# Performance work log

Hardware: AMD Instinct MI355X
Metric: run time of the kernel (lower is better)

The kernel has to match this reference:

```python
import jax, jax.numpy as jnp
import numpy as np

N = 100000
IN_DIM = 256
HID = 128
E = 1600000


def _gcn_conv(x, W, b, src, dst, n_nodes):
    """PyG GCNConv: add self-loops, symmetric normalization, linear transform."""
    xw = x @ W  # [N, H]
    loop = jnp.arange(n_nodes, dtype=src.dtype)
    s = jnp.concatenate([src, loop])  # sources (j)
    d = jnp.concatenate([dst, loop])  # targets (i)
    ones = jnp.ones(s.shape[0], dtype=x.dtype)
    deg = jax.ops.segment_sum(ones, d, num_segments=n_nodes)  # in-degree incl. self-loop
    dinv = jnp.where(deg > 0, jax.lax.rsqrt(deg), 0.0)
    norm = dinv[s] * dinv[d]  # [E+N]
    msgs = xw[s] * norm[:, None]  # gather + scale
    out = jax.ops.segment_sum(msgs, d, num_segments=n_nodes)  # scatter-add at targets
    return out + b


def setup_inputs() -> dict:
    key = jax.random.key(0)
    ks = jax.random.split(key, 12)
    x = jax.random.normal(ks[0], (N, IN_DIM), dtype=jnp.float32)
    edge_index = jax.random.randint(ks[1], (2, E), 0, N, dtype=jnp.int64)
    h_node = jax.random.uniform(ks[2], (N,), dtype=jnp.float32)
    # learned params (glorot-ish scale)
    W1 = jax.random.normal(ks[3], (IN_DIM, HID), dtype=jnp.float32) / np.sqrt(IN_DIM)
    b1 = jnp.zeros((HID,), dtype=jnp.float32)
    W2 = jax.random.normal(ks[4], (HID, HID), dtype=jnp.float32) / np.sqrt(HID)
    b2 = jnp.zeros((HID,), dtype=jnp.float32)
    Wc = jax.random.normal(ks[5], (HID, 2), dtype=jnp.float32) / np.sqrt(HID)
    bc = jnp.zeros((2,), dtype=jnp.float32)
    Wf = jax.random.normal(ks[6], (HID, 2), dtype=jnp.float32) / np.sqrt(HID)
    bf = jnp.zeros((2,), dtype=jnp.float32)
    return {"x": x, "edge_index": edge_index, "h_node": h_node,
            "W1": W1, "b1": b1, "W2": W2, "b2": b2,
            "Wc": Wc, "bc": bc, "Wf": Wf, "bf": bf}


def reference(x, edge_index, h_node, W1, b1, W2, b2, Wc, bc, Wf, bf):
    src, dst = edge_index[0], edge_index[1]
    h1 = jax.nn.relu(_gcn_conv(x, W1, b1, src, dst, x.shape[0]))      # [N, HID]
    logits_coarse = h1 @ Wc + bc                                      # [N, 2]
    alpha = h_node[:, None]                                           # [N, 1]
    h2 = jax.nn.relu(_gcn_conv(h1, W2, b2, src, dst, x.shape[0]))     # [N, HID]
    h2_adaptive = alpha * h2 + (1.0 - alpha) * h1
    logits_fine = h2_adaptive @ Wf + bf                               # [N, 2]
    return 0.5 * logits_coarse + 0.5 * logits_fine
```

## Files before the change

### kernel.cpp

```cpp
#include <hip/hip_runtime.h>


#define HID 128
#define SHIFT 9
#define RANGE 512
#define MAXB 256
#define TILE 4096

typedef __bf16 bf16x8 __attribute__((ext_vector_type(8)));
typedef float  f32x4  __attribute__((ext_vector_type(4)));

__device__ __forceinline__ unsigned short f2bf(float x) {
    unsigned int b = __float_as_uint(x);
    b += 0x7fffu + ((b >> 16) & 1u);
    return (unsigned short)(b >> 16);
}
__device__ __forceinline__ float bflo(unsigned int u) { return __uint_as_float(u << 16); }
__device__ __forceinline__ float bfhi(unsigned int u) { return __uint_as_float(u & 0xffff0000u); }
__device__ __forceinline__ unsigned packbf(float a, float b) {
    return (unsigned)f2bf(a) | ((unsigned)f2bf(b) << 16);
}

__device__ __forceinline__ void gload_lds16(const void* g, void* l) {
    __builtin_amdgcn_global_load_lds(
        (const __attribute__((address_space(1))) void*)g,
        (__attribute__((address_space(3))) void*)l, 16, 0, 0);
}


__global__ __launch_bounds__(256)
void bincount_kernel(const int* __restrict__ dst, int* __restrict__ bin_counts,
                     int E, int NB) {
    __shared__ int h[MAXB];
    for (int i = threadIdx.x; i < NB; i += 256) h[i] = 0;
    __syncthreads();
    const int base = blockIdx.x * TILE;
#pragma unroll
    for (int j = 0; j < TILE; j += 256) {
        int e = base + j + threadIdx.x;
        if (e < E) atomicAdd(&h[((unsigned)dst[e]) >> SHIFT], 1);
    }
    __syncthreads();
    for (int i = threadIdx.x; i < NB; i += 256) {
        int v = h[i];
        if (v) atomicAdd(&bin_counts[i], v);
    }
}

__global__ void binscan_kernel(const int* __restrict__ bin_counts,
                               int* __restrict__ bin_off, int* __restrict__ bin_cur, int NB) {
    __shared__ int sh[MAXB];
    const int t = threadIdx.x;
    int v = (t < NB) ? bin_counts[t] : 0;
    sh[t] = v;
    __syncthreads();
    for (int s = 1; s < 256; s <<= 1) {
        int x = (t >= s) ? sh[t - s] : 0;
        __syncthreads();
        sh[t] += x;
        __syncthreads();
    }
    if (t < NB) {
        int ex = sh[t] - v;
        bin_off[t] = ex;
        bin_cur[t] = ex;
    }
}

__global__ __launch_bounds__(256)
void stage_kernel(const int* __restrict__ src, const int* __restrict__ dst,
                  int* __restrict__ bin_cur, unsigned* __restrict__ pairs, int E) {
    __shared__ int sh_hist[MAXB];
    __shared__ int sh_off[MAXB];
    __shared__ int sh_ex[MAXB];
    __shared__ int sh_gbase[MAXB];
    __shared__ uint2 stg[TILE];
    const int t = threadIdx.x;
    const int base = blockIdx.x * TILE;
    const int cnt = min(TILE, E - base);

    for (int i = t; i < MAXB; i += 256) sh_hist[i] = 0;
    __syncthreads();

    int s[16], d[16], r[16];
#pragma unroll
    for (int j = 0; j < 16; ++j) {
        const int k = j * 256 + t;
        if (k < cnt) {
            s[j] = src[base + k];
            d[j] = dst[base + k];
            r[j] = atomicAdd(&sh_hist[((unsigned)d[j]) >> SHIFT], 1);
        }
    }
    __syncthreads();

    const int hv = sh_hist[t];
    sh_off[t] = hv;
    __syncthreads();
    for (int st = 1; st < 256; st <<= 1) {
        int x = (t >= st) ? sh_off[t - st] : 0;
        __syncthreads();
        sh_off[t] += x;
        __syncthreads();
    }
    sh_ex[t] = sh_off[t] - hv;
    if (hv > 0) sh_gbase[t] = atomicAdd(&bin_cur[t], hv);
    __syncthreads();

#pragma unroll
    for (int j = 0; j < 16; ++j) {
        const int k = j * 256 + t;
        if (k < cnt) {
            int b = ((unsigned)d[j]) >> SHIFT;
            stg[sh_ex[b] + r[j]] = make_uint2((unsigned)s[j], (unsigned)d[j]);
        }
    }
    __syncthreads();

    for (int i = t; i < cnt; i += 256) {
        uint2 p = stg[i];
        int b = (int)(p.y >> SHIFT);
        unsigned w = ((p.y & (RANGE - 1)) << 23) | p.x;
        pairs[sh_gbase[b] + (i - sh_ex[b])] = w;
    }
}

__global__ __launch_bounds__(256)
void binrowp_kernel(const unsigned* __restrict__ pairs, const int* __restrict__ bin_off,
                    float* __restrict__ dinv, int* __restrict__ rowp,
                    int N, int NB, int E) {
    __shared__ int c[RANGE];
    __shared__ int sh[256];
    const int b = blockIdx.x;
    const int t = threadIdx.x;
    const int nb = b << SHIFT;
    const int nr = min(RANGE, N - nb);
    for (int i = t; i < RANGE; i += 256) c[i] = 0;
    __syncthreads();
    const int lo = bin_off[b];
    const int hi = (b + 1 < NB) ? bin_off[b + 1] : E;
    for (int i = lo + t; i < hi; i += 256)
        atomicAdd(&c[pairs[i] >> 23], 1);
    __syncthreads();
    const int v0 = c[2 * t], v1 = c[2 * t + 1];
    const int pr = v0 + v1;
    sh[t] = pr;
    __syncthreads();
    for (int s = 1; s < 256; s <<= 1) {
        int x = (t >= s) ? sh[t - s] : 0;
        __syncthreads();
        sh[t] += x;
        __syncthreads();
    }
    const int ex = sh[t] - pr + lo;
    if (2 * t < nr) {
        rowp[nb + 2 * t] = ex;
        dinv[nb + 2 * t] = rsqrtf((float)(v0 + 1));
    }
    if (2 * t + 1 < nr) {
        rowp[nb + 2 * t + 1] = ex + v0;
        dinv[nb + 2 * t + 1] = rsqrtf((float)(v1 + 1));
    }
    if (b == 0 && t == 0) rowp[N] = E;
}

__global__ __launch_bounds__(256)
void fine_kernel(const unsigned* __restrict__ pairs, const int* __restrict__ bin_off,
                 const int* __restrict__ rowp, const float* __restrict__ dinv,
                 uint2* __restrict__ colv2, int N, int NB, int E) {
    __shared__ int cur[RANGE];
    const int b = blockIdx.x;
    const int nb = b << SHIFT;
    const int nr = min(RANGE, N - nb);
    for (int i = threadIdx.x; i < nr; i += 256) cur[i] = rowp[nb + i];
    __syncthreads();
    const int lo = bin_off[b];
    const int hi = (b + 1 < NB) ? bin_off[b + 1] : E;
    for (int i = lo + threadIdx.x; i < hi; i += 256) {
        unsigned w = pairs[i];
        unsigned s = w & 0x7fffffu;
        int pos = atomicAdd(&cur[w >> 23], 1);
        colv2[pos] = make_uint2(s, __float_as_uint(dinv[s]));
    }
}

__global__ void wtprep_kernel(const float* __restrict__ W, unsigned short* __restrict__ Wt, int K) {
    int idx = blockIdx.x * 256 + threadIdx.x;
    if (idx < 128 * K) {
        int nn = idx / K, k = idx - nn * K;
        Wt[(size_t)nn * K + k] = f2bf(W[(size_t)k * 128 + nn]);
    }
}

template <bool A_BF16>
__global__ __launch_bounds__(256)
void gemm_kernel(const void* __restrict__ Aptr, const unsigned short* __restrict__ Wt,
                 unsigned short* __restrict__ Out, int nrows, int K) {
    __shared__ __align__(16) char tilebuf[16384];
    const int tid  = threadIdx.x;
    const int wave = tid >> 6;
    const int lane = tid & 63;
    const int q = lane >> 4;
    const int r = lane & 15;
    const int blkrow = blockIdx.x * 128;
    const int wrow = blkrow + wave * 32;

    f32x4 acc[2][8];
#pragma unroll
    for (int s = 0; s < 2; ++s)
#pragma unroll
        for (int c = 0; c < 8; ++c) acc[s][c] = (f32x4){0.f, 0.f, 0.f, 0.f};

    for (int k0 = 0; k0 < K; k0 += 32) {
        if (A_BF16) {
            const unsigned short* A = (const unsigned short*)Aptr;
#pragma unroll
            for (int c = 0; c < 2; ++c) {
                const int u = tid + c * 256;
                const int l = u & 63;
                const int g = u >> 6;
                int row = blkrow + (g >> 1) * 32 + (g & 1) * 16 + (l & 15);
                row = min(row, nrows - 1);
                const int k = k0 + (l >> 4) * 8;
                gload_lds16(A + (size_t)row * K + k,
                            tilebuf + c * 4096 + wave * 1024);
            }
        } else {
            const float* A = (const float*)Aptr;
#pragma unroll
            for (int c = 0; c < 4; ++c) {
                const int u = tid + c * 256;
                const int l = u & 63;
                const int g = u >> 6;
                const int half = g & 1;
                const int ws = g >> 1;
                int row = blkrow + (ws >> 1) * 32 + (ws & 1) * 16 + (l & 15);
                row = min(row, nrows - 1);
                const int k = k0 + (l >> 4) * 8 + half * 4;
                gload_lds16(A + (size_t)row * K + k,
                            tilebuf + c * 4096 + wave * 1024);
            }
        }
        __syncthreads();

        const int kk = k0 + q * 8;
        bf16x8 afrag[2];
#pragma unroll
        for (int s = 0; s < 2; ++s) {
            if (A_BF16) {
                afrag[s] = *reinterpret_cast<const bf16x8*>(
                    tilebuf + ((wave * 2 + s) * 64 + lane) * 16);
            } else {
                const float4 x0 = *reinterpret_cast<const float4*>(
                    tilebuf + (((wave * 2 + s) * 2 + 0) * 64 + lane) * 16);
                const float4 x1 = *reinterpret_cast<const float4*>(
                    tilebuf + (((wave * 2 + s) * 2 + 1) * 64 + lane) * 16);
                bf16x8 a;
                a[0] = (__bf16)x0.x; a[1] = (__bf16)x0.y; a[2] = (__bf16)x0.z; a[3] = (__bf16)x0.w;
                a[4] = (__bf16)x1.x; a[5] = (__bf16)x1.y; a[6] = (__bf16)x1.z; a[7] = (__bf16)x1.w;
                afrag[s] = a;
            }
        }
#pragma unroll
        for (int c = 0; c < 8; ++c) {
            const bf16x8 b = *reinterpret_cast<const bf16x8*>(Wt + (size_t)(c * 16 + r) * K + kk);
#pragma unroll
            for (int s = 0; s < 2; ++s)
                acc[s][c] = __builtin_amdgcn_mfma_f32_16x16x32_bf16(afrag[s], b, acc[s][c], 0, 0, 0);
        }
        __syncthreads();
    }
#pragma unroll
    for (int s = 0; s < 2; ++s)
#pragma unroll
        for (int v = 0; v < 4; ++v) {
            const int row = wrow + s * 16 + q * 4 + v;
            if (row < nrows) {
#pragma unroll
                for (int c = 0; c < 8; ++c)
                    Out[(size_t)row * 128 + c * 16 + r] = f2bf(acc[s][c][v]);
            }
        }
}


__global__ __launch_bounds__(256)
void agg1_kernel(const uint4* __restrict__ xw, const uint2* __restrict__ colv2,
                 const int* __restrict__ rowp, const float* __restrict__ dinv,
                 const float* __restrict__ b1, const float* __restrict__ Wc,
                 const float* __restrict__ bc, uint4* __restrict__ h1,
                 float* __restrict__ outp, int n) {
    const int node = blockIdx.x * 4 + (threadIdx.x >> 6);
    if (node >= n) return;
    const int lane = threadIdx.x & 63;
    const int c    = lane & 15;
    const int q4   = lane >> 4;
    const float di = dinv[node];

    float a0=0.f,a1=0.f,a2=0.f,a3=0.f,a4=0.f,a5=0.f,a6=0.f,a7=0.f;
    {
        const float ws = (q4 == 0) ? di : 0.f;
        const uint4 uu = xw[((unsigned)node << 4) + c];
        a0 += bflo(uu.x)*ws; a1 += bfhi(uu.x)*ws;
        a2 += bflo(uu.y)*ws; a3 += bfhi(uu.y)*ws;
        a4 += bflo(uu.z)*ws; a5 += bfhi(uu.z)*ws;
        a6 += bflo(uu.w)*ws; a7 += bfhi(uu.w)*ws;
    }

    const int beg = rowp[node], end = rowp[node + 1];
    for (int base = beg; base < end; base += 64) {
        const int e = base + lane;
        unsigned s = 0; float w = 0.f;
        if (e < end) { uint2 cw = colv2[e]; s = cw.x; w = __uint_as_float(cw.y); }
        const int cnt = min(64, end - base);
#pragma unroll 4
        for (int t = 0; t < cnt; t += 4) {
            const unsigned st = (unsigned)__shfl((int)s, t + q4);
            const float    wt = __shfl(w, t + q4);
            const uint4 uu = xw[(st << 4) + c];
            a0 += bflo(uu.x)*wt; a1 += bfhi(uu.x)*wt;
            a2 += bflo(uu.y)*wt; a3 += bfhi(uu.y)*wt;
            a4 += bflo(uu.z)*wt; a5 += bfhi(uu.z)*wt;
            a6 += bflo(uu.w)*wt; a7 += bfhi(uu.w)*wt;
        }
    }
    a0 += __shfl_xor(a0,16); a1 += __shfl_xor(a1,16);
    a2 += __shfl_xor(a2,16); a3 += __shfl_xor(a3,16);
    a4 += __shfl_xor(a4,16); a5 += __shfl_xor(a5,16);
    a6 += __shfl_xor(a6,16); a7 += __shfl_xor(a7,16);
    a0 += __shfl_xor(a0,32); a1 += __shfl_xor(a1,32);
    a2 += __shfl_xor(a2,32); a3 += __shfl_xor(a3,32);
    a4 += __shfl_xor(a4,32); a5 += __shfl_xor(a5,32);
    a6 += __shfl_xor(a6,32); a7 += __shfl_xor(a7,32);

    const float4 bb0 = reinterpret_cast<const float4*>(b1)[2*c];
    const float4 bb1 = reinterpret_cast<const float4*>(b1)[2*c + 1];
    a0 = fmaxf(a0*di + bb0.x, 0.f);  a1 = fmaxf(a1*di + bb0.y, 0.f);
    a2 = fmaxf(a2*di + bb0.z, 0.f);  a3 = fmaxf(a3*di + bb0.w, 0.f);
    a4 = fmaxf(a4*di + bb1.x, 0.f);  a5 = fmaxf(a5*di + bb1.y, 0.f);
    a6 = fmaxf(a6*di + bb1.z, 0.f);  a7 = fmaxf(a7*di + bb1.w, 0.f);

    if (q4 == 0)
        h1[((unsigned)node << 4) + c] =
            make_uint4(packbf(a0,a1), packbf(a2,a3), packbf(a4,a5), packbf(a6,a7));

    const float4 w0 = reinterpret_cast<const float4*>(Wc)[4*c];
    const float4 w1 = reinterpret_cast<const float4*>(Wc)[4*c + 1];
    const float4 w2 = reinterpret_cast<const float4*>(Wc)[4*c + 2];
    const float4 w3 = reinterpret_cast<const float4*>(Wc)[4*c + 3];
    float c0 = a0*w0.x + a1*w0.z + a2*w1.x + a3*w1.z
             + a4*w2.x + a5*w2.z + a6*w3.x + a7*w3.z;
    float c1 = a0*w0.y + a1*w0.w + a2*w1.y + a3*w1.w
             + a4*w2.y + a5*w2.w + a6*w3.y + a7*w3.w;
    if (q4) { c0 = 0.f; c1 = 0.f; }
#pragma unroll
    for (int off = 32; off; off >>= 1) {
        c0 += __shfl_down(c0, off);
        c1 += __shfl_down(c1, off);
    }
    if (lane == 0) {
        outp[2 * (size_t)node]     = 0.5f * (c0 + bc[0]);
        outp[2 * (size_t)node + 1] = 0.5f * (c1 + bc[1]);
    }
}

__global__ __launch_bounds__(256)
void agg2_kernel(const uint4* __restrict__ xw2, const uint4* __restrict__ h1,
                 const uint2* __restrict__ colv2, const int* __restrict__ rowp,
                 const float* __restrict__ dinv, const float* __restrict__ b2,
                 const float* __restrict__ Wf, const float* __restrict__ bfv,
                 const float* __restrict__ hnode, float* __restrict__ outp, int n) {
    const int node = blockIdx.x * 4 + (threadIdx.x >> 6);
    if (node >= n) return;
    const int lane = threadIdx.x & 63;
    const int c    = lane & 15;
    const int q4   = lane >> 4;
    const float di = dinv[node];

    float a0=0.f,a1=0.f,a2=0.f,a3=0.f,a4=0.f,a5=0.f,a6=0.f,a7=0.f;
    {
        const float ws = (q4 == 0) ? di : 0.f;
        const uint4 uu = xw2[((unsigned)node << 4) + c];
        a0 += bflo(uu.x)*ws; a1 += bfhi(uu.x)*ws;
        a2 += bflo(uu.y)*ws; a3 += bfhi(uu.y)*ws;
        a4 += bflo(uu.z)*ws; a5 += bfhi(uu.z)*ws;
        a6 += bflo(uu.w)*ws; a7 += bfhi(uu.w)*ws;
    }

    const int beg = rowp[node], end = rowp[node + 1];
    for (int base = beg; base < end; base += 64) {
        const int e = base + lane;
        unsigned s = 0; float w = 0.f;
        if (e < end) { uint2 cw = colv2[e]; s = cw.x; w = __uint_as_float(cw.y); }
        const int cnt = min(64, end - base);
#pragma unroll 4
        for (int t = 0; t < cnt; t += 4) {
            const unsigned st = (unsigned)__shfl((int)s, t + q4);
            const float    wt = __shfl(w, t + q4);
            const uint4 uu = xw2[(st << 4) + c];
            a0 += bflo(uu.x)*wt; a1 += bfhi(uu.x)*wt;
            a2 += bflo(uu.y)*wt; a3 += bfhi(uu.y)*wt;
            a4 += bflo(uu.z)*wt; a5 += bfhi(uu.z)*wt;
            a6 += bflo(uu.w)*wt; a7 += bfhi(uu.w)*wt;
        }
    }
    a0 += __shfl_xor(a0,16); a1 += __shfl_xor(a1,16);
    a2 += __shfl_xor(a2,16); a3 += __shfl_xor(a3,16);
    a4 += __shfl_xor(a4,16); a5 += __shfl_xor(a5,16);
    a6 += __shfl_xor(a6,16); a7 += __shfl_xor(a7,16);
    a0 += __shfl_xor(a0,32); a1 += __shfl_xor(a1,32);
    a2 += __shfl_xor(a2,32); a3 += __shfl_xor(a3,32);
    a4 += __shfl_xor(a4,32); a5 += __shfl_xor(a5,32);
    a6 += __shfl_xor(a6,32); a7 += __shfl_xor(a7,32);

    const float4 bb0 = reinterpret_cast<const float4*>(b2)[2*c];
    const float4 bb1 = reinterpret_cast<const float4*>(b2)[2*c + 1];
    float h20 = fmaxf(a0*di + bb0.x, 0.f);  float h21 = fmaxf(a1*di + bb0.y, 0.f);
    float h22 = fmaxf(a2*di + bb0.z, 0.f);  float h23 = fmaxf(a3*di + bb0.w, 0.f);
    float h24 = fmaxf(a4*di + bb1.x, 0.f);  float h25 = fmaxf(a5*di + bb1.y, 0.f);
    float h26 = fmaxf(a6*di + bb1.z, 0.f);  float h27 = fmaxf(a7*di + bb1.w, 0.f);

    const float alpha = hnode[node];
    const float beta  = 1.f - alpha;
    const uint4 hh = h1[((unsigned)node << 4) + c];
    const float ha0 = alpha*h20 + beta*bflo(hh.x);
    const float ha1 = alpha*h21 + beta*bfhi(hh.x);
    const float ha2 = alpha*h22 + beta*bflo(hh.y);
    const float ha3 = alpha*h23 + beta*bfhi(hh.y);
    const float ha4 = alpha*h24 + beta*bflo(hh.z);
    const float ha5 = alpha*h25 + beta*bfhi(hh.z);
    const float ha6 = alpha*h26 + beta*bflo(hh.w);
    const float ha7 = alpha*h27 + beta*bfhi(hh.w);

    const float4 w0 = reinterpret_cast<const float4*>(Wf)[4*c];
    const float4 w1 = reinterpret_cast<const float4*>(Wf)[4*c + 1];
    const float4 w2 = reinterpret_cast<const float4*>(Wf)[4*c + 2];
    const float4 w3 = reinterpret_cast<const float4*>(Wf)[4*c + 3];
    float f0 = ha0*w0.x + ha1*w0.z + ha2*w1.x + ha3*w1.z
             + ha4*w2.x + ha5*w2.z + ha6*w3.x + ha7*w3.z;
    float f1 = ha0*w0.y + ha1*w0.w + ha2*w1.y + ha3*w1.w
             + ha4*w2.y + ha5*w2.w + ha6*w3.y + ha7*w3.w;
    if (q4) { f0 = 0.f; f1 = 0.f; }
#pragma unroll
    for (int off = 32; off; off >>= 1) {
        f0 += __shfl_down(f0, off);
        f1 += __shfl_down(f1, off);
    }
    if (lane == 0) {
        outp[2 * (size_t)node]     += 0.5f * (f0 + bfv[0]);
        outp[2 * (size_t)node + 1] += 0.5f * (f1 + bfv[1]);
    }
}


extern "C" void kernel_launch(void* const* d_in, const int* in_sizes, int n_in,
                              void* d_out, int out_size, void* d_ws, size_t ws_size,
                              hipStream_t stream) {
    const float* x     = (const float*)d_in[0];
    const int*   ei    = (const int*)d_in[1];
    const float* hnode = (const float*)d_in[2];
    const float* W1    = (const float*)d_in[3];
    const float* b1    = (const float*)d_in[4];
    const float* W2    = (const float*)d_in[5];
    const float* b2    = (const float*)d_in[6];
    const float* Wc    = (const float*)d_in[7];
    const float* bc    = (const float*)d_in[8];
    const float* Wf    = (const float*)d_in[9];
    const float* bfv   = (const float*)d_in[10];

    const int N  = in_sizes[2];
    const int E  = in_sizes[1] / 2;
    const int K1 = in_sizes[3] / HID;
    const int NB = (N + RANGE - 1) >> SHIFT;
    const int* srcv = ei;
    const int* dstv = ei + E;
    float* outp = (float*)d_out;

    char* ws = (char*)d_ws;
    size_t off = 0;
    auto alloc = [&](size_t bytes) -> char* {
        char* p = ws + off;
        off += (bytes + 255) & ~(size_t)255;
        return p;
    };
    unsigned short* xw       = (unsigned short*)alloc((size_t)N * HID * 2);
    unsigned short* h1       = (unsigned short*)alloc((size_t)N * HID * 2);
    float*          dinv     = (float*)alloc((size_t)N * 4);
    int*            rowp     = (int*)alloc((size_t)(N + 1) * 4);
    uint2*          colv2    = (uint2*)alloc((size_t)E * 8);
    unsigned*       pairs    = (unsigned*)alloc((size_t)E * 4);
    int*            bin_counts = (int*)alloc(MAXB * 4);
    int*            bin_off    = (int*)alloc(MAXB * 4);
    int*            bin_cur    = (int*)alloc(MAXB * 4);
    unsigned short* wt1      = (unsigned short*)alloc((size_t)HID * K1 * 2);
    unsigned short* wt2      = (unsigned short*)alloc((size_t)HID * HID * 2);

    hipMemsetAsync(bin_counts, 0, MAXB * 4, stream);
    wtprep_kernel<<<(HID * K1 + 255) / 256, 256, 0, stream>>>(W1, wt1, K1);
    wtprep_kernel<<<(HID * HID + 255) / 256, 256, 0, stream>>>(W2, wt2, HID);

    const int ntiles = (E + TILE - 1) / TILE;
    bincount_kernel<<<ntiles, 256, 0, stream>>>(dstv, bin_counts, E, NB);
    binscan_kernel<<<1, 256, 0, stream>>>(bin_counts, bin_off, bin_cur, NB);
    stage_kernel<<<ntiles, 256, 0, stream>>>(srcv, dstv, bin_cur, pairs, E);
    binrowp_kernel<<<NB, 256, 0, stream>>>(pairs, bin_off, dinv, rowp, N, NB, E);
    fine_kernel<<<NB, 256, 0, stream>>>(pairs, bin_off, rowp, dinv, colv2, N, NB, E);

    gemm_kernel<false><<<(N + 127) / 128, 256, 0, stream>>>((const void*)x, wt1, xw, N, K1);
    agg1_kernel<<<(N + 3) / 4, 256, 0, stream>>>((const uint4*)xw, colv2, rowp, dinv,
                                                 b1, Wc, bc, (uint4*)h1, outp, N);
    gemm_kernel<true><<<(N + 127) / 128, 256, 0, stream>>>((const void*)h1, wt2, xw, N, HID);
    agg2_kernel<<<(N + 3) / 4, 256, 0, stream>>>((const uint4*)xw, (const uint4*)h1, colv2,
                                                 rowp, dinv, b2, Wf, bfv, hnode, outp, N);
}
```

Before: 450.4 us.

## Pack edge source and quantized weight into one 32-bit word, fuse prep kernels

The CSR column array now stores each edge as a single 32-bit word: a 17-bit source index shifted left by 15 bits and the source's dinv quantized to 15 bits. This replaces the 8-byte uint2 and halves edge-list traffic in fine_kernel and both aggregation kernels. The two weight-transpose kernels and the bin_counts memset are merged into one launch, and the accumulators use float2 vectors with byte-offset addressing. The 15-bit weight quantization adds numeric error, and the packing limits node count to 2^17.

```diff
diff --git a/kernel.cpp b/kernel.cpp
--- a/kernel.cpp
+++ b/kernel.cpp
@@ -9,6 +9,7 @@
 
 typedef __bf16 bf16x8 __attribute__((ext_vector_type(8)));
 typedef float  f32x4  __attribute__((ext_vector_type(4)));
+typedef float  f32x2  __attribute__((ext_vector_type(2)));
 
 __device__ __forceinline__ unsigned short f2bf(float x) {
     unsigned int b = __float_as_uint(x);
@@ -167,7 +168,7 @@
 __global__ __launch_bounds__(256)
 void fine_kernel(const unsigned* __restrict__ pairs, const int* __restrict__ bin_off,
                  const int* __restrict__ rowp, const float* __restrict__ dinv,
-                 uint2* __restrict__ colv2, int N, int NB, int E) {
+                 unsigned* __restrict__ colv1, int N, int NB, int E) {
     __shared__ int cur[RANGE];
     const int b = blockIdx.x;
     const int nb = b << SHIFT;
@@ -180,15 +181,23 @@
         unsigned w = pairs[i];
         unsigned s = w & 0x7fffffu;
         int pos = atomicAdd(&cur[w >> 23], 1);
-        colv2[pos] = make_uint2(s, __float_as_uint(dinv[s]));
-    }
-}
-
-__global__ void wtprep_kernel(const float* __restrict__ W, unsigned short* __restrict__ Wt, int K) {
+        unsigned w15 = __float2uint_rn(dinv[s] * 32767.0f);
+        colv1[pos] = (s << 15) | w15;
+    }
+}
+
+__global__ void prep_kernel(const float* __restrict__ W1, const float* __restrict__ W2,
+                            unsigned short* __restrict__ wt1, unsigned short* __restrict__ wt2,
+                            int K1, int* __restrict__ bin_counts) {
     int idx = blockIdx.x * 256 + threadIdx.x;
-    if (idx < 128 * K) {
-        int nn = idx / K, k = idx - nn * K;
-        Wt[(size_t)nn * K + k] = f2bf(W[(size_t)k * 128 + nn]);
+    if (idx < MAXB) bin_counts[idx] = 0;
+    if (idx < 128 * K1) {
+        int nn = idx / K1, k = idx - nn * K1;
+        wt1[(size_t)nn * K1 + k] = f2bf(W1[(size_t)k * 128 + nn]);
+    }
+    if (idx < 128 * 128) {
+        int nn = idx >> 7, k = idx & 127;
+        wt2[(size_t)nn * 128 + k] = f2bf(W2[(size_t)k * 128 + nn]);
     }
 }
 
@@ -284,8 +293,35 @@
 }
 
 
-__global__ __launch_bounds__(256)
-void agg1_kernel(const uint4* __restrict__ xw, const uint2* __restrict__ colv2,
+#define AGG_EDGE_LOOP(XW)                                                      \
+    for (int base = beg; base < end; base += 64) {                             \
+        const int e = base + lane;                                             \
+        const unsigned cw = (e < end) ? colv1[e] : 0u;                         \
+        const int cnt = min(64, end - base);                                   \
+        _Pragma("unroll 4")                                                    \
+        for (int t = 0; t < cnt; t += 4) {                                     \
+            const unsigned cg = (unsigned)__shfl((int)cw, t + q4);             \
+            const unsigned st = cg >> 15;                                      \
+            const float    wt = (float)(cg & 0x7fffu) * (1.0f / 32767.0f);     \
+            const uint4 uu = *reinterpret_cast<const uint4*>(                  \
+                (const char*)(XW) + ((st << 8) + coff));                       \
+            A0 += (f32x2){bflo(uu.x), bfhi(uu.x)} * wt;                        \
+            A1 += (f32x2){bflo(uu.y), bfhi(uu.y)} * wt;                        \
+            A2 += (f32x2){bflo(uu.z), bfhi(uu.z)} * wt;                        \
+            A3 += (f32x2){bflo(uu.w), bfhi(uu.w)} * wt;                        \
+        }                                                                      \
+    }                                                                          \
+    A0 += __shfl_xor(A0, 16); A1 += __shfl_xor(A1, 16);                        \
+    A2 += __shfl_xor(A2, 16); A3 += __shfl_xor(A3, 16);                        \
+    A0 += __shfl_xor(A0, 32); A1 += __shfl_xor(A1, 32);                        \
+    A2 += __shfl_xor(A2, 32); A3 += __shfl_xor(A3, 32);
+
+__device__ __forceinline__ f32x2 __shfl_xor(f32x2 v, int m) {
+    return (f32x2){__shfl_xor(v[0], m), __shfl_xor(v[1], m)};
+}
+
+__global__ __launch_bounds__(256)
+void agg1_kernel(const unsigned short* __restrict__ xw, const unsigned* __restrict__ colv1,
                  const int* __restrict__ rowp, const float* __restrict__ dinv,
                  const float* __restrict__ b1, const float* __restrict__ Wc,
                  const float* __restrict__ bc, uint4* __restrict__ h1,
@@ -295,50 +331,29 @@
     const int lane = threadIdx.x & 63;
     const int c    = lane & 15;
     const int q4   = lane >> 4;
+    const unsigned coff = (unsigned)c << 4;
     const float di = dinv[node];
 
-    float a0=0.f,a1=0.f,a2=0.f,a3=0.f,a4=0.f,a5=0.f,a6=0.f,a7=0.f;
+    f32x2 A0 = {0.f,0.f}, A1 = {0.f,0.f}, A2 = {0.f,0.f}, A3 = {0.f,0.f};
     {
         const float ws = (q4 == 0) ? di : 0.f;
-        const uint4 uu = xw[((unsigned)node << 4) + c];
-        a0 += bflo(uu.x)*ws; a1 += bfhi(uu.x)*ws;
-        a2 += bflo(uu.y)*ws; a3 += bfhi(uu.y)*ws;
-        a4 += bflo(uu.z)*ws; a5 += bfhi(uu.z)*ws;
-        a6 += bflo(uu.w)*ws; a7 += bfhi(uu.w)*ws;
+        const uint4 uu = *reinterpret_cast<const uint4*>(
+            (const char*)xw + (((unsigned)node << 8) + coff));
+        A0 += (f32x2){bflo(uu.x), bfhi(uu.x)} * ws;
+        A1 += (f32x2){bflo(uu.y), bfhi(uu.y)} * ws;
+        A2 += (f32x2){bflo(uu.z), bfhi(uu.z)} * ws;
+        A3 += (f32x2){bflo(uu.w), bfhi(uu.w)} * ws;
     }
 
     const int beg = rowp[node], end = rowp[node + 1];
-    for (int base = beg; base < end; base += 64) {
-        const int e = base + lane;
-        unsigned s = 0; float w = 0.f;
-        if (e < end) { uint2 cw = colv2[e]; s = cw.x; w = __uint_as_float(cw.y); }
-        const int cnt = min(64, end - base);
-#pragma unroll 4
-        for (int t = 0; t < cnt; t += 4) {
-            const unsigned st = (unsigned)__shfl((int)s, t + q4);
-            const float    wt = __shfl(w, t + q4);
-            const uint4 uu = xw[(st << 4) + c];
-            a0 += bflo(uu.x)*wt; a1 += bfhi(uu.x)*wt;
-            a2 += bflo(uu.y)*wt; a3 += bfhi(uu.y)*wt;
-            a4 += bflo(uu.z)*wt; a5 += bfhi(uu.z)*wt;
-            a6 += bflo(uu.w)*wt; a7 += bfhi(uu.w)*wt;
-        }
-    }
-    a0 += __shfl_xor(a0,16); a1 += __shfl_xor(a1,16);
-    a2 += __shfl_xor(a2,16); a3 += __shfl_xor(a3,16);
-    a4 += __shfl_xor(a4,16); a5 += __shfl_xor(a5,16);
-    a6 += __shfl_xor(a6,16); a7 += __shfl_xor(a7,16);
-    a0 += __shfl_xor(a0,32); a1 += __shfl_xor(a1,32);
-    a2 += __shfl_xor(a2,32); a3 += __shfl_xor(a3,32);
-    a4 += __shfl_xor(a4,32); a5 += __shfl_xor(a5,32);
-    a6 += __shfl_xor(a6,32); a7 += __shfl_xor(a7,32);
+    AGG_EDGE_LOOP(xw)
 
     const float4 bb0 = reinterpret_cast<const float4*>(b1)[2*c];
     const float4 bb1 = reinterpret_cast<const float4*>(b1)[2*c + 1];
-    a0 = fmaxf(a0*di + bb0.x, 0.f);  a1 = fmaxf(a1*di + bb0.y, 0.f);
-    a2 = fmaxf(a2*di + bb0.z, 0.f);  a3 = fmaxf(a3*di + bb0.w, 0.f);
-    a4 = fmaxf(a4*di + bb1.x, 0.f);  a5 = fmaxf(a5*di + bb1.y, 0.f);
-    a6 = fmaxf(a6*di + bb1.z, 0.f);  a7 = fmaxf(a7*di + bb1.w, 0.f);
+    float a0 = fmaxf(A0[0]*di + bb0.x, 0.f), a1 = fmaxf(A0[1]*di + bb0.y, 0.f);
+    float a2 = fmaxf(A1[0]*di + bb0.z, 0.f), a3 = fmaxf(A1[1]*di + bb0.w, 0.f);
+    float a4 = fmaxf(A2[0]*di + bb1.x, 0.f), a5 = fmaxf(A2[1]*di + bb1.y, 0.f);
+    float a6 = fmaxf(A3[0]*di + bb1.z, 0.f), a7 = fmaxf(A3[1]*di + bb1.w, 0.f);
 
     if (q4 == 0)
         h1[((unsigned)node << 4) + c] =
@@ -365,8 +380,8 @@
 }
 
 __global__ __launch_bounds__(256)
-void agg2_kernel(const uint4* __restrict__ xw2, const uint4* __restrict__ h1,
-                 const uint2* __restrict__ colv2, const int* __restrict__ rowp,
+void agg2_kernel(const unsigned short* __restrict__ xw2, const uint4* __restrict__ h1,
+                 const unsigned* __restrict__ colv1, const int* __restrict__ rowp,
                  const float* __restrict__ dinv, const float* __restrict__ b2,
                  const float* __restrict__ Wf, const float* __restrict__ bfv,
                  const float* __restrict__ hnode, float* __restrict__ outp, int n) {
@@ -375,50 +390,29 @@
     const int lane = threadIdx.x & 63;
     const int c    = lane & 15;
     const int q4   = lane >> 4;
+    const unsigned coff = (unsigned)c << 4;
     const float di = dinv[node];
 
-    float a0=0.f,a1=0.f,a2=0.f,a3=0.f,a4=0.f,a5=0.f,a6=0.f,a7=0.f;
+    f32x2 A0 = {0.f,0.f}, A1 = {0.f,0.f}, A2 = {0.f,0.f}, A3 = {0.f,0.f};
     {
         const float ws = (q4 == 0) ? di : 0.f;
-        const uint4 uu = xw2[((unsigned)node << 4) + c];
-        a0 += bflo(uu.x)*ws; a1 += bfhi(uu.x)*ws;
-        a2 += bflo(uu.y)*ws; a3 += bfhi(uu.y)*ws;
-        a4 += bflo(uu.z)*ws; a5 += bfhi(uu.z)*ws;
-        a6 += bflo(uu.w)*ws; a7 += bfhi(uu.w)*ws;
+        const uint4 uu = *reinterpret_cast<const uint4*>(
+            (const char*)xw2 + (((unsigned)node << 8) + coff));
+        A0 += (f32x2){bflo(uu.x), bfhi(uu.x)} * ws;
+        A1 += (f32x2){bflo(uu.y), bfhi(uu.y)} * ws;
+        A2 += (f32x2){bflo(uu.z), bfhi(uu.z)} * ws;
+        A3 += (f32x2){bflo(uu.w), bfhi(uu.w)} * ws;
     }
 
     const int beg = rowp[node], end = rowp[node + 1];
-    for (int base = beg; base < end; base += 64) {
-        const int e = base + lane;
-        unsigned s = 0; float w = 0.f;
-        if (e < end) { uint2 cw = colv2[e]; s = cw.x; w = __uint_as_float(cw.y); }
-        const int cnt = min(64, end - base);
-#pragma unroll 4
-        for (int t = 0; t < cnt; t += 4) {
-            const unsigned st = (unsigned)__shfl((int)s, t + q4);
-            const float    wt = __shfl(w, t + q4);
-            const uint4 uu = xw2[(st << 4) + c];
-            a0 += bflo(uu.x)*wt; a1 += bfhi(uu.x)*wt;
-            a2 += bflo(uu.y)*wt; a3 += bfhi(uu.y)*wt;
-            a4 += bflo(uu.z)*wt; a5 += bfhi(uu.z)*wt;
-            a6 += bflo(uu.w)*wt; a7 += bfhi(uu.w)*wt;
-        }
-    }
-    a0 += __shfl_xor(a0,16); a1 += __shfl_xor(a1,16);
-    a2 += __shfl_xor(a2,16); a3 += __shfl_xor(a3,16);
-    a4 += __shfl_xor(a4,16); a5 += __shfl_xor(a5,16);
-    a6 += __shfl_xor(a6,16); a7 += __shfl_xor(a7,16);
-    a0 += __shfl_xor(a0,32); a1 += __shfl_xor(a1,32);
-    a2 += __shfl_xor(a2,32); a3 += __shfl_xor(a3,32);
-    a4 += __shfl_xor(a4,32); a5 += __shfl_xor(a5,32);
-    a6 += __shfl_xor(a6,32); a7 += __shfl_xor(a7,32);
+    AGG_EDGE_LOOP(xw2)
 
     const float4 bb0 = reinterpret_cast<const float4*>(b2)[2*c];
     const float4 bb1 = reinterpret_cast<const float4*>(b2)[2*c + 1];
-    float h20 = fmaxf(a0*di + bb0.x, 0.f);  float h21 = fmaxf(a1*di + bb0.y, 0.f);
-    float h22 = fmaxf(a2*di + bb0.z, 0.f);  float h23 = fmaxf(a3*di + bb0.w, 0.f);
-    float h24 = fmaxf(a4*di + bb1.x, 0.f);  float h25 = fmaxf(a5*di + bb1.y, 0.f);
-    float h26 = fmaxf(a6*di + bb1.z, 0.f);  float h27 = fmaxf(a7*di + bb1.w, 0.f);
+    float h20 = fmaxf(A0[0]*di + bb0.x, 0.f), h21 = fmaxf(A0[1]*di + bb0.y, 0.f);
+    float h22 = fmaxf(A1[0]*di + bb0.z, 0.f), h23 = fmaxf(A1[1]*di + bb0.w, 0.f);
+    float h24 = fmaxf(A2[0]*di + bb1.x, 0.f), h25 = fmaxf(A2[1]*di + bb1.y, 0.f);
+    float h26 = fmaxf(A3[0]*di + bb1.z, 0.f), h27 = fmaxf(A3[1]*di + bb1.w, 0.f);
 
     const float alpha = hnode[node];
     const float beta  = 1.f - alpha;
@@ -487,7 +481,7 @@
     unsigned short* h1       = (unsigned short*)alloc((size_t)N * HID * 2);
     float*          dinv     = (float*)alloc((size_t)N * 4);
     int*            rowp     = (int*)alloc((size_t)(N + 1) * 4);
-    uint2*          colv2    = (uint2*)alloc((size_t)E * 8);
+    unsigned*       colv1    = (unsigned*)alloc((size_t)E * 4);
     unsigned*       pairs    = (unsigned*)alloc((size_t)E * 4);
     int*            bin_counts = (int*)alloc(MAXB * 4);
     int*            bin_off    = (int*)alloc(MAXB * 4);
@@ -495,21 +489,19 @@
     unsigned short* wt1      = (unsigned short*)alloc((size_t)HID * K1 * 2);
     unsigned short* wt2      = (unsigned short*)alloc((size_t)HID * HID * 2);
 
-    hipMemsetAsync(bin_counts, 0, MAXB * 4, stream);
-    wtprep_kernel<<<(HID * K1 + 255) / 256, 256, 0, stream>>>(W1, wt1, K1);
-    wtprep_kernel<<<(HID * HID + 255) / 256, 256, 0, stream>>>(W2, wt2, HID);
+    prep_kernel<<<(HID * K1 + 255) / 256, 256, 0, stream>>>(W1, W2, wt1, wt2, K1, bin_counts);
 
     const int ntiles = (E + TILE - 1) / TILE;
     bincount_kernel<<<ntiles, 256, 0, stream>>>(dstv, bin_counts, E, NB);
     binscan_kernel<<<1, 256, 0, stream>>>(bin_counts, bin_off, bin_cur, NB);
     stage_kernel<<<ntiles, 256, 0, stream>>>(srcv, dstv, bin_cur, pairs, E);
     binrowp_kernel<<<NB, 256, 0, stream>>>(pairs, bin_off, dinv, rowp, N, NB, E);
-    fine_kernel<<<NB, 256, 0, stream>>>(pairs, bin_off, rowp, dinv, colv2, N, NB, E);
+    fine_kernel<<<NB, 256, 0, stream>>>(pairs, bin_off, rowp, dinv, colv1, N, NB, E);
 
     gemm_kernel<false><<<(N + 127) / 128, 256, 0, stream>>>((const void*)x, wt1, xw, N, K1);
-    agg1_kernel<<<(N + 3) / 4, 256, 0, stream>>>((const uint4*)xw, colv2, rowp, dinv,
+    agg1_kernel<<<(N + 3) / 4, 256, 0, stream>>>(xw, colv1, rowp, dinv,
                                                  b1, Wc, bc, (uint4*)h1, outp, N);
     gemm_kernel<true><<<(N + 127) / 128, 256, 0, stream>>>((const void*)h1, wt2, xw, N, HID);
-    agg2_kernel<<<(N + 3) / 4, 256, 0, stream>>>((const uint4*)xw, (const uint4*)h1, colv2,
+    agg2_kernel<<<(N + 3) / 4, 256, 0, stream>>>(xw, (const uint4*)h1, colv1,
                                                  rowp, dinv, b2, Wf, bfv, hnode, outp, N);
 }
```

After: 445.7 us. About the same (-1.1%).
